# Kernel tuning notes

Measured on AMD Instinct MI355X. Metric: run time of the kernel, lower is better.

The kernel has to match this reference:

```python
import jax, jax.numpy as jnp
import numpy as np

# IO parameters (aihwkit-style preset)
INP_BOUND = 1.0
INP_RES = 1.0 / 254.0      # 8-bit DAC: 2^8 - 2 levels
OUT_BOUND = 12.0
OUT_RES = 1.0 / 510.0      # 9-bit ADC: 2^9 - 2 levels
OUT_NOISE = 0.06
OUT_SCALE = 1.0
MAX_BM_FACTOR = 1000.0
MAX_BM_RES = 0.25
INP_RES_EFF = 2.0 * INP_BOUND * INP_RES  # effective input grid step (bm escape test)


def _quantize_st(x, res, bound):
    # UniformQuantize: round to grid of step (res * 2 * bound), straight-through grad
    r = (1.0 / res if res > 1.0 else res) * 2.0 * bound
    q = jnp.round(x / r) * r
    return x + jax.lax.stop_gradient(q - x)


def _one_pass(input_, weight, nm, reduction, rnd, key):
    """One analog MVM pass at a given bound-management reduction factor."""
    scale = 1.0 / (nm * reduction)                      # [m, 1]
    x = input_ * scale                                  # noise/bound managed input
    x = _quantize_st(x, INP_RES, INP_BOUND)             # DAC discretization
    x = jnp.clip(x, -INP_BOUND, INP_BOUND)              # DAC clipping
    out = x @ weight.T                                  # [m, out_size] analog GEMM
    noise = OUT_NOISE * jax.random.normal(
        jax.random.fold_in(key, rnd), out.shape, out.dtype)
    out = out + noise                                   # output (ADC) noise
    out = _quantize_st(out, OUT_RES, OUT_BOUND)         # ADC discretization
    not_clipping = jnp.all((out <= OUT_BOUND) & (out >= -OUT_BOUND))
    out = jnp.clip(out, -OUT_BOUND, OUT_BOUND)          # ADC saturation
    return not_clipping, out


def setup_inputs() -> dict:
    key = jax.random.key(0)
    k1, k2 = jax.random.split(key)
    input_ = jax.random.normal(k1, (8192, 4096), jnp.float32)
    # 0.1 std weights -> outputs mostly within ADC bound after 1-2 bm rounds
    weight = 0.1 * jax.random.normal(k2, (4096, 4096), jnp.float32)
    return {"input_": input_, "weight": weight}


def reference(input_, weight):
    key = jax.random.key(42)
    # noise management: ABS_MAX over the input dimension (nm_thres <= 0 -> no clamp)
    nm = jnp.max(jnp.abs(input_), axis=-1, keepdims=True)
    nm = jnp.where(nm <= 0.0, 1.0, nm)
    out_shape = input_.shape[:-1] + (weight.shape[0],)

    def cond(c):
        return ~c[2]

    def body(c):
        rnd, red, _, _ = c
        red = red * 2.0          # reduction_due_to_bound_management *= 2
        rnd = rnd + 1
        passed, out = _one_pass(input_, weight, nm, red, rnd, key)
        passed = passed | (red > MAX_BM_FACTOR) | (red > MAX_BM_RES / INP_RES_EFF)
        return (rnd, red, passed, out)

    init = (jnp.int32(0), jnp.float32(0.5), jnp.array(False),
            jnp.zeros(out_shape, input_.dtype))
    _, red, _, out = jax.lax.while_loop(cond, body, init)
    # undo the input scaling: output *= out_scale / scale = out_scale * nm * red
    return out * (OUT_SCALE * nm * red)
```

## Files before the change

kernel.cpp:

```cpp
#include <hip/hip_runtime.h>
#include <stdint.h>


#define MM 8192
#define KK 4096
#define NN 4096
#define TOTAL_OUT ((size_t)MM * (size_t)NN)
#define GEMM_BLOCKS 2048

typedef __attribute__((ext_vector_type(4))) float f32x4;
typedef __attribute__((ext_vector_type(8))) short bf16x8;
typedef __attribute__((ext_vector_type(8))) unsigned short u16x8;

#define R_IN_F ((float)(2.0 / 254.0))
#define R_OUT_F ((float)(24.0 / 510.0))

struct BmState {
  int done;
  float red_final;
  int viol[8];
  int ctr[8];
};

__host__ __device__ __forceinline__ uint32_t tf_rotl(uint32_t v, int r) {
  return (v << r) | (v >> (32 - r));
}

__host__ __device__ __forceinline__ void threefry2x32(uint32_t k0, uint32_t k1,
                                                      uint32_t x0, uint32_t x1,
                                                      uint32_t &o0, uint32_t &o1) {
  uint32_t ks2 = k0 ^ k1 ^ 0x1BD11BDAu;
  x0 += k0; x1 += k1;
#define TF_R(r) { x0 += x1; x1 = tf_rotl(x1, r); x1 ^= x0; }
  TF_R(13) TF_R(15) TF_R(26) TF_R(6)
  x0 += k1; x1 += ks2 + 1u;
  TF_R(17) TF_R(29) TF_R(16) TF_R(24)
  x0 += ks2; x1 += k0 + 2u;
  TF_R(13) TF_R(15) TF_R(26) TF_R(6)
  x0 += k0; x1 += k1 + 3u;
  TF_R(17) TF_R(29) TF_R(16) TF_R(24)
  x0 += k1; x1 += ks2 + 4u;
  TF_R(13) TF_R(15) TF_R(26) TF_R(6)
  x0 += ks2; x1 += k0 + 5u;
#undef TF_R
  o0 = x0; o1 = x1;
}

__device__ __forceinline__ float erfinv_xla(float x) {
  float w = -log1pf(-x * x);
  float p;
  if (w < 5.0f) {
    w = w - 2.5f;
    p = 2.81022636e-08f;
    p = fmaf(p, w, 3.43273939e-07f);
    p = fmaf(p, w, -3.5233877e-06f);
    p = fmaf(p, w, -4.39150654e-06f);
    p = fmaf(p, w, 0.00021858087f);
    p = fmaf(p, w, -0.00125372503f);
    p = fmaf(p, w, -0.00417768164f);
    p = fmaf(p, w, 0.246640727f);
    p = fmaf(p, w, 1.50140941f);
  } else {
    w = sqrtf(w) - 3.0f;
    p = -0.000200214257f;
    p = fmaf(p, w, 0.000100950558f);
    p = fmaf(p, w, 0.00134934322f);
    p = fmaf(p, w, -0.00367342844f);
    p = fmaf(p, w, 0.00573950773f);
    p = fmaf(p, w, -0.0076224613f);
    p = fmaf(p, w, 0.00943887047f);
    p = fmaf(p, w, 1.00167406f);
    p = fmaf(p, w, 2.83297682f);
  }
  return p * x;
}

__device__ __forceinline__ float noise_from_bits(uint32_t bits) {
  uint32_t fb = (bits >> 9) | 0x3f800000u;
  float f = __uint_as_float(fb) - 1.0f;
  const float lo = -0.99999994f;
  float u = f * 2.0f + lo;
  u = fmaxf(lo, u);
  return 0.06f * (1.41421356f * erfinv_xla(u));
}

__device__ __forceinline__ unsigned short bf16_rne(float f) {
  uint32_t x = __float_as_uint(f);
  x += 0x7fffu + ((x >> 16) & 1u);
  return (unsigned short)(x >> 16);
}

__device__ __forceinline__ float dac_quant(float v, float s) {
  float x = v * s;
  float t = x / R_IN_F;
  float k = rintf(t);
  return fminf(127.0f, fmaxf(-127.0f, k));
}

__device__ __forceinline__ u16x8 quant8(float4 a, float4 b, float s) {
  u16x8 o;
  o[0] = bf16_rne(dac_quant(a.x, s));
  o[1] = bf16_rne(dac_quant(a.y, s));
  o[2] = bf16_rne(dac_quant(a.z, s));
  o[3] = bf16_rne(dac_quant(a.w, s));
  o[4] = bf16_rne(dac_quant(b.x, s));
  o[5] = bf16_rne(dac_quant(b.y, s));
  o[6] = bf16_rne(dac_quant(b.z, s));
  o[7] = bf16_rne(dac_quant(b.w, s));
  return o;
}

__device__ __forceinline__ u16x8 conv8(float4 a, float4 b) {
  u16x8 o;
  o[0] = bf16_rne(a.x); o[1] = bf16_rne(a.y); o[2] = bf16_rne(a.z); o[3] = bf16_rne(a.w);
  o[4] = bf16_rne(b.x); o[5] = bf16_rne(b.y); o[6] = bf16_rne(b.z); o[7] = bf16_rne(b.w);
  return o;
}

__device__ __forceinline__ float adc_one(float gval, size_t idx, float sc,
                                         uint32_t fk0, uint32_t fk1, bool &bad) {
  uint32_t w0, w1;
  threefry2x32(fk0, fk1, 0u, (uint32_t)idx, w0, w1);
  float o = R_IN_F * gval + noise_from_bits(w0 ^ w1);
  float q = rintf(o / R_OUT_F) * R_OUT_F;
  float z = o + (q - o);
  bad = bad || (z > 12.0f) || (z < -12.0f);
  z = fminf(12.0f, fmaxf(-12.0f, z));
  return z * sc;
}

__device__ __forceinline__ void fin_tail(BmState *st, int pass, float red, int nblocks,
                                         bool bad) {
  unsigned long long vb = __ballot(bad ? 1 : 0);
  if (vb != 0ull && (threadIdx.x & 63) == 0) atomicOr(&st->viol[pass], 1);
  __syncthreads();
  if (threadIdx.x == 0) {
    __threadfence();
    int prev = atomicAdd(&st->ctr[pass], 1);
    if (prev == nblocks - 1) {
      int viol = atomicOr(&st->viol[pass], 0);
      bool ok = (viol == 0) || (red > 1000.0f) || (red > 31.75f);
      if (ok) {
        st->done = 1;
        st->red_final = red;
      }
    }
  }
}

__global__ __launch_bounds__(256) void k_rowmax(const float *__restrict__ in,
                                                float *__restrict__ nm, BmState *st) {
  if (blockIdx.x == 0 && threadIdx.x == 0) {
    st->done = 0;
    st->red_final = 0.0f;
    for (int i = 0; i < 8; ++i) { st->viol[i] = 0; st->ctr[i] = 0; }
  }
  const int row = blockIdx.x;
  const float4 *r = (const float4 *)(in + (size_t)row * KK);
  const int t = threadIdx.x;
  float m = 0.0f;
#pragma unroll
  for (int i = 0; i < 4; ++i) {
    float4 v = r[t + i * 256];
    m = fmaxf(m, fmaxf(fmaxf(fabsf(v.x), fabsf(v.y)), fmaxf(fabsf(v.z), fabsf(v.w))));
  }
#pragma unroll
  for (int off = 32; off > 0; off >>= 1) m = fmaxf(m, __shfl_down(m, off));
  __shared__ float wm[4];
  if ((t & 63) == 0) wm[t >> 6] = m;
  __syncthreads();
  if (t == 0) {
    m = fmaxf(fmaxf(wm[0], wm[1]), fmaxf(wm[2], wm[3]));
    nm[row] = (m <= 0.0f) ? 1.0f : m;
  }
}

__global__ __launch_bounds__(256) void k_wconv(const float *__restrict__ w,
                                               unsigned short *__restrict__ wb) {
  const size_t idx = ((size_t)blockIdx.x * 256 + threadIdx.x) * 8;
  float4 a = *(const float4 *)(w + idx);
  float4 b = *(const float4 *)(w + idx + 4);
  *(u16x8 *)(wb + idx) = conv8(a, b);
}

__global__ __launch_bounds__(256) void k_quant(const float *__restrict__ in,
                                               const float *__restrict__ nm,
                                               unsigned short *__restrict__ ab) {
  const size_t idx = ((size_t)blockIdx.x * 256 + threadIdx.x) * 8;
  const int row = (int)(idx >> 12);
  const float s = 1.0f / (nm[row] * 1.0f);
  float4 a = *(const float4 *)(in + idx);
  float4 b = *(const float4 *)(in + idx + 4);
  *(u16x8 *)(ab + idx) = quant8(a, b, s);
}

__device__ __forceinline__ void async16(const void *g, void *l) {
  __builtin_amdgcn_global_load_lds((const __attribute__((address_space(1))) uint32_t *)g,
                                   (__attribute__((address_space(3))) uint32_t *)l,
                                   16, 0, 0);
}

__global__ __launch_bounds__(256) void k_gemm(const unsigned short *__restrict__ A,
                                              const unsigned short *__restrict__ B,
                                              float *__restrict__ C) {
  __shared__ unsigned short As[128 * 64];
  __shared__ unsigned short Bs[128 * 64];
  const int tid = threadIdx.x;
  const int lane = tid & 63;
  const int wv = tid >> 6;
  const int wr = wv >> 1, wc = wv & 1;
  const int brow = blockIdx.y * 128;
  const int bcol = blockIdx.x * 128;

  f32x4 acc[4][4];
#pragma unroll
  for (int m = 0; m < 4; ++m)
#pragma unroll
    for (int n = 0; n < 4; ++n) acc[m][n] = (f32x4){0.f, 0.f, 0.f, 0.f};

  for (int kt = 0; kt < KK; kt += 64) {
#pragma unroll
    for (int i = 0; i < 4; ++i) {
      const int u0 = i * 256 + wv * 64;
      const int u = u0 + lane;
      const int r = u >> 3;
      const int cg = (u & 7) ^ (r & 7);
      const int k8 = cg * 8;
      async16(A + (size_t)(brow + r) * KK + kt + k8, (char *)As + (size_t)u0 * 16);
      async16(B + (size_t)(bcol + r) * KK + kt + k8, (char *)Bs + (size_t)u0 * 16);
    }
    __syncthreads();

    const int r16 = lane & 15;
    const int kg = (lane >> 4) * 8;
#pragma unroll
    for (int kk = 0; kk < 64; kk += 32) {
      const int ck = (kk + kg) >> 3;
      bf16x8 af[4], bg[4];
#pragma unroll
      for (int m = 0; m < 4; ++m) {
        const int ra = wr * 64 + m * 16 + r16;
        af[m] = *(const bf16x8 *)(As + ra * 64 + ((ck ^ (ra & 7)) << 3));
      }
#pragma unroll
      for (int n = 0; n < 4; ++n) {
        const int rb = wc * 64 + n * 16 + r16;
        bg[n] = *(const bf16x8 *)(Bs + rb * 64 + ((ck ^ (rb & 7)) << 3));
      }
#pragma unroll
      for (int m = 0; m < 4; ++m)
#pragma unroll
        for (int n = 0; n < 4; ++n)
          acc[m][n] = __builtin_amdgcn_mfma_f32_16x16x32_bf16(af[m], bg[n], acc[m][n], 0, 0, 0);
    }
    __syncthreads();
  }

  const int c16 = lane & 15;
  const int q4 = (lane >> 4) * 4;
#pragma unroll
  for (int m = 0; m < 4; ++m) {
    const int row = brow + wr * 64 + m * 16 + q4;
#pragma unroll
    for (int n = 0; n < 4; ++n) {
      const int col = bcol + wc * 64 + n * 16 + c16;
      float *cp = C + (size_t)row * NN + col;
      cp[0 * (size_t)NN] = acc[m][n][0];
      cp[1 * (size_t)NN] = acc[m][n][1];
      cp[2 * (size_t)NN] = acc[m][n][2];
      cp[3 * (size_t)NN] = acc[m][n][3];
    }
  }
}

__global__ __launch_bounds__(256) void k_epi(float *__restrict__ out,
                                             const float *__restrict__ nm,
                                             BmState *__restrict__ st, int pass, float red,
                                             uint32_t fk0, uint32_t fk1) {
  const size_t idx = ((size_t)blockIdx.x * 256 + threadIdx.x) * 8;
  const int row = (int)(idx >> 12);
  const float sc = nm[row] * red;
  float4 a = *(const float4 *)(out + idx);
  float4 b = *(const float4 *)(out + idx + 4);
  float v[8] = {a.x, a.y, a.z, a.w, b.x, b.y, b.z, b.w};
  bool bad = false;
#pragma unroll
  for (int j = 0; j < 8; ++j) v[j] = adc_one(v[j], idx + j, sc, fk0, fk1, bad);
  *(float4 *)(out + idx) = make_float4(v[0], v[1], v[2], v[3]);
  *(float4 *)(out + idx + 4) = make_float4(v[4], v[5], v[6], v[7]);
  unsigned long long vb = __ballot(bad ? 1 : 0);
  if (vb != 0ull && (threadIdx.x & 63) == 0) atomicOr(&st->viol[pass], 1);
}

__global__ void k_fin(BmState *st, int pass, float red) {
  if (st->done) return;
  bool ok = (st->viol[pass] == 0) || (red > 1000.0f) || (red > 31.75f);
  if (ok) {
    st->done = 1;
    st->red_final = red;
  }
}

__global__ __launch_bounds__(256) void k_retry(const float *__restrict__ Af,
                                               const float *__restrict__ Bf,
                                               const float *__restrict__ nm, float red,
                                               float *__restrict__ C,
                                               BmState *__restrict__ st, int pass,
                                               uint32_t fk0, uint32_t fk1) {
  if (st->done) return;
  __shared__ unsigned short As[128 * 64];
  __shared__ unsigned short Bs[128 * 64];
  const int tid = threadIdx.x;
  const int lane = tid & 63;
  const int wv = tid >> 6;
  const int wr = wv >> 1, wc = wv & 1;
  const int brow = blockIdx.y * 128;
  const int bcol = blockIdx.x * 128;

  f32x4 acc[4][4];
#pragma unroll
  for (int m = 0; m < 4; ++m)
#pragma unroll
    for (int n = 0; n < 4; ++n) acc[m][n] = (f32x4){0.f, 0.f, 0.f, 0.f};

  float sA[4];
#pragma unroll
  for (int i = 0; i < 4; ++i) {
    int u = i * 256 + tid;
    sA[i] = 1.0f / (nm[brow + (u >> 3)] * red);
  }

  for (int kt = 0; kt < KK; kt += 64) {
#pragma unroll
    for (int i = 0; i < 4; ++i) {
      const int u = i * 256 + tid;
      const int r = u >> 3, k8 = (u & 7) * 8;
      {
        const float *g = Af + (size_t)(brow + r) * KK + kt + k8;
        float4 x = *(const float4 *)g, y = *(const float4 *)(g + 4);
        *(u16x8 *)(As + r * 64 + k8) = quant8(x, y, sA[i]);
      }
      {
        const float *g = Bf + (size_t)(bcol + r) * KK + kt + k8;
        float4 x = *(const float4 *)g, y = *(const float4 *)(g + 4);
        *(u16x8 *)(Bs + r * 64 + k8) = conv8(x, y);
      }
    }
    __syncthreads();

    const int r16 = lane & 15;
    const int kg = (lane >> 4) * 8;
#pragma unroll
    for (int kk = 0; kk < 64; kk += 32) {
      bf16x8 af[4], bg[4];
#pragma unroll
      for (int m = 0; m < 4; ++m)
        af[m] = *(const bf16x8 *)(As + (wr * 64 + m * 16 + r16) * 64 + kk + kg);
#pragma unroll
      for (int n = 0; n < 4; ++n)
        bg[n] = *(const bf16x8 *)(Bs + (wc * 64 + n * 16 + r16) * 64 + kk + kg);
#pragma unroll
      for (int m = 0; m < 4; ++m)
#pragma unroll
        for (int n = 0; n < 4; ++n)
          acc[m][n] = __builtin_amdgcn_mfma_f32_16x16x32_bf16(af[m], bg[n], acc[m][n], 0, 0, 0);
    }
    __syncthreads();
  }

  const int c16 = lane & 15;
  const int q4 = (lane >> 4) * 4;
  bool bad = false;
#pragma unroll
  for (int m = 0; m < 4; ++m) {
    const int row0 = brow + wr * 64 + m * 16 + q4;
#pragma unroll
    for (int j = 0; j < 4; ++j) {
      const int row = row0 + j;
      const float sc = nm[row] * red;
#pragma unroll
      for (int n = 0; n < 4; ++n) {
        const int col = bcol + wc * 64 + n * 16 + c16;
        const size_t idx = (size_t)row * NN + col;
        C[idx] = adc_one(acc[m][n][j], idx, sc, fk0, fk1, bad);
      }
    }
  }
  fin_tail(st, pass, red, GEMM_BLOCKS, bad);
}

extern "C" void kernel_launch(void *const *d_in, const int *in_sizes, int n_in,
                              void *d_out, int out_size, void *d_ws, size_t ws_size,
                              hipStream_t stream) {
  const float *input = (const float *)d_in[0];
  const float *weight = (const float *)d_in[1];
  if (n_in >= 2 && in_sizes[0] < in_sizes[1]) {
    const float *t = input; input = weight; weight = t;
  }
  float *out = (float *)d_out;
  char *ws = (char *)d_ws;
  BmState *st = (BmState *)ws;
  float *nm = (float *)(ws + 4096);
  unsigned short *Ab = (unsigned short *)(ws + 36864);
  unsigned short *Wb = Ab + (size_t)MM * KK;
  const size_t need = 36864 + ((size_t)MM * KK + (size_t)NN * KK) * 2;
  const bool fast = ws_size >= need;

  uint32_t fk[8][2];
  for (int p = 1; p <= 6; ++p) threefry2x32(0u, 42u, 0u, (uint32_t)p, fk[p][0], fk[p][1]);

  k_rowmax<<<dim3(MM), dim3(256), 0, stream>>>(input, nm, st);

  if (fast) {
    k_wconv<<<dim3((NN * (size_t)KK) / 2048), dim3(256), 0, stream>>>(weight, Wb);
    k_quant<<<dim3((MM * (size_t)KK) / 2048), dim3(256), 0, stream>>>(input, nm, Ab);
    k_gemm<<<dim3(NN / 128, MM / 128), dim3(256), 0, stream>>>(Ab, Wb, out);
    k_epi<<<dim3((int)(TOTAL_OUT / 2048)), dim3(256), 0, stream>>>(out, nm, st, 1, 1.0f,
                                                                   fk[1][0], fk[1][1]);
    k_fin<<<dim3(1), dim3(1), 0, stream>>>(st, 1, 1.0f);
  } else {
    k_retry<<<dim3(NN / 128, MM / 128), dim3(256), 0, stream>>>(
        input, weight, nm, 1.0f, out, st, 1, fk[1][0], fk[1][1]);
  }

  float red = 2.0f;
  for (int p = 2; p <= 6; ++p, red *= 2.0f) {
    k_retry<<<dim3(NN / 128, MM / 128), dim3(256), 0, stream>>>(
        input, weight, nm, red, out, st, p, fk[p][0], fk[p][1]);
  }
}
```

Before: 557.0 us.

## Double-buffer GEMM LDS tiles and fuse row-max with input quantization

The GEMM now keeps two LDS buffers for A and B. It issues the async global-to-LDS loads for the next K tile before computing the current one, using explicit vmcnt waits and barriers, so load latency is hidden behind the MFMA work. The separate row-max and quantize kernels are also merged into one per-row kernel that reads each input row once, which removes one full pass over the input and one launch. The cost is double the LDS per block, which may reduce occupancy, plus more fragile hand-written wait-count synchronization.

```diff
diff --git a/kernel.cpp b/kernel.cpp
--- a/kernel.cpp
+++ b/kernel.cpp
@@ -7,6 +7,7 @@
 #define NN 4096
 #define TOTAL_OUT ((size_t)MM * (size_t)NN)
 #define GEMM_BLOCKS 2048
+#define NT (KK / 64)
 
 typedef __attribute__((ext_vector_type(4))) float f32x4;
 typedef __attribute__((ext_vector_type(8))) short bf16x8;
@@ -148,6 +149,41 @@
   }
 }
 
+__global__ __launch_bounds__(256) void k_rowquant(const float *__restrict__ in,
+                                                  float *__restrict__ nm,
+                                                  unsigned short *__restrict__ ab,
+                                                  BmState *st) {
+  if (blockIdx.x == 0 && threadIdx.x == 0) {
+    st->done = 0;
+    st->red_final = 0.0f;
+    for (int i = 0; i < 8; ++i) { st->viol[i] = 0; st->ctr[i] = 0; }
+  }
+  const int row = blockIdx.x;
+  const float *r = in + (size_t)row * KK;
+  const int t = threadIdx.x;
+  float4 a0 = *(const float4 *)(r + t * 8);
+  float4 a1 = *(const float4 *)(r + t * 8 + 4);
+  float4 b0 = *(const float4 *)(r + 2048 + t * 8);
+  float4 b1 = *(const float4 *)(r + 2048 + t * 8 + 4);
+  float m = 0.0f;
+  m = fmaxf(m, fmaxf(fmaxf(fabsf(a0.x), fabsf(a0.y)), fmaxf(fabsf(a0.z), fabsf(a0.w))));
+  m = fmaxf(m, fmaxf(fmaxf(fabsf(a1.x), fabsf(a1.y)), fmaxf(fabsf(a1.z), fabsf(a1.w))));
+  m = fmaxf(m, fmaxf(fmaxf(fabsf(b0.x), fabsf(b0.y)), fmaxf(fabsf(b0.z), fabsf(b0.w))));
+  m = fmaxf(m, fmaxf(fmaxf(fabsf(b1.x), fabsf(b1.y)), fmaxf(fabsf(b1.z), fabsf(b1.w))));
+#pragma unroll
+  for (int off = 32; off > 0; off >>= 1) m = fmaxf(m, __shfl_down(m, off));
+  __shared__ float wm[4];
+  if ((t & 63) == 0) wm[t >> 6] = m;
+  __syncthreads();
+  const float mm = fmaxf(fmaxf(wm[0], wm[1]), fmaxf(wm[2], wm[3]));
+  const float nmv = (mm <= 0.0f) ? 1.0f : mm;
+  if (t == 0) nm[row] = nmv;
+  const float s = 1.0f / (nmv * 1.0f);
+  unsigned short *o = ab + (size_t)row * KK;
+  *(u16x8 *)(o + t * 8) = quant8(a0, a1, s);
+  *(u16x8 *)(o + 2048 + t * 8) = quant8(b0, b1, s);
+}
+
 __global__ __launch_bounds__(256) void k_rowmax(const float *__restrict__ in,
                                                 float *__restrict__ nm, BmState *st) {
   if (blockIdx.x == 0 && threadIdx.x == 0) {
@@ -183,17 +219,6 @@
   *(u16x8 *)(wb + idx) = conv8(a, b);
 }
 
-__global__ __launch_bounds__(256) void k_quant(const float *__restrict__ in,
-                                               const float *__restrict__ nm,
-                                               unsigned short *__restrict__ ab) {
-  const size_t idx = ((size_t)blockIdx.x * 256 + threadIdx.x) * 8;
-  const int row = (int)(idx >> 12);
-  const float s = 1.0f / (nm[row] * 1.0f);
-  float4 a = *(const float4 *)(in + idx);
-  float4 b = *(const float4 *)(in + idx + 4);
-  *(u16x8 *)(ab + idx) = quant8(a, b, s);
-}
-
 __device__ __forceinline__ void async16(const void *g, void *l) {
   __builtin_amdgcn_global_load_lds((const __attribute__((address_space(1))) uint32_t *)g,
                                    (__attribute__((address_space(3))) uint32_t *)l,
@@ -203,8 +228,8 @@
 __global__ __launch_bounds__(256) void k_gemm(const unsigned short *__restrict__ A,
                                               const unsigned short *__restrict__ B,
                                               float *__restrict__ C) {
-  __shared__ unsigned short As[128 * 64];
-  __shared__ unsigned short Bs[128 * 64];
+  __shared__ unsigned short As[2][128 * 64];
+  __shared__ unsigned short Bs[2][128 * 64];
   const int tid = threadIdx.x;
   const int lane = tid & 63;
   const int wv = tid >> 6;
@@ -218,21 +243,42 @@
 #pragma unroll
     for (int n = 0; n < 4; ++n) acc[m][n] = (f32x4){0.f, 0.f, 0.f, 0.f};
 
-  for (int kt = 0; kt < KK; kt += 64) {
-#pragma unroll
-    for (int i = 0; i < 4; ++i) {
-      const int u0 = i * 256 + wv * 64;
-      const int u = u0 + lane;
-      const int r = u >> 3;
-      const int cg = (u & 7) ^ (r & 7);
-      const int k8 = cg * 8;
-      async16(A + (size_t)(brow + r) * KK + kt + k8, (char *)As + (size_t)u0 * 16);
-      async16(B + (size_t)(bcol + r) * KK + kt + k8, (char *)Bs + (size_t)u0 * 16);
-    }
-    __syncthreads();
-
-    const int r16 = lane & 15;
-    const int kg = (lane >> 4) * 8;
+  const int su0[4] = {0 * 256 + wv * 64, 1 * 256 + wv * 64, 2 * 256 + wv * 64,
+                      3 * 256 + wv * 64};
+  int sr[4], sk8[4];
+#pragma unroll
+  for (int i = 0; i < 4; ++i) {
+    const int u = su0[i] + lane;
+    sr[i] = u >> 3;
+    sk8[i] = ((u & 7) ^ (sr[i] & 7)) * 8;
+  }
+
+#define STAGE(buf, kt)                                                                 \
+  {                                                                                    \
+    _Pragma("unroll") for (int i = 0; i < 4; ++i) {                                    \
+      async16(A + (size_t)(brow + sr[i]) * KK + (kt) * 64 + sk8[i],                    \
+              (char *)As[buf] + (size_t)su0[i] * 16);                                  \
+      async16(B + (size_t)(bcol + sr[i]) * KK + (kt) * 64 + sk8[i],                    \
+              (char *)Bs[buf] + (size_t)su0[i] * 16);                                  \
+    }                                                                                  \
+  }
+
+  STAGE(0, 0);
+
+  const int r16 = lane & 15;
+  const int kg = (lane >> 4) * 8;
+
+#pragma unroll 2
+  for (int kt = 0; kt < NT; ++kt) {
+    const int cur = kt & 1;
+    if (kt + 1 < NT) {
+      STAGE(cur ^ 1, kt + 1);
+      asm volatile("s_waitcnt vmcnt(8)" ::: "memory");
+    } else {
+      asm volatile("s_waitcnt vmcnt(0)" ::: "memory");
+    }
+    __builtin_amdgcn_s_barrier();
+
 #pragma unroll
     for (int kk = 0; kk < 64; kk += 32) {
       const int ck = (kk + kg) >> 3;
@@ -240,12 +286,12 @@
 #pragma unroll
       for (int m = 0; m < 4; ++m) {
         const int ra = wr * 64 + m * 16 + r16;
-        af[m] = *(const bf16x8 *)(As + ra * 64 + ((ck ^ (ra & 7)) << 3));
+        af[m] = *(const bf16x8 *)(As[cur] + ra * 64 + ((ck ^ (ra & 7)) << 3));
       }
 #pragma unroll
       for (int n = 0; n < 4; ++n) {
         const int rb = wc * 64 + n * 16 + r16;
-        bg[n] = *(const bf16x8 *)(Bs + rb * 64 + ((ck ^ (rb & 7)) << 3));
+        bg[n] = *(const bf16x8 *)(Bs[cur] + rb * 64 + ((ck ^ (rb & 7)) << 3));
       }
 #pragma unroll
       for (int m = 0; m < 4; ++m)
@@ -253,8 +299,10 @@
         for (int n = 0; n < 4; ++n)
           acc[m][n] = __builtin_amdgcn_mfma_f32_16x16x32_bf16(af[m], bg[n], acc[m][n], 0, 0, 0);
     }
-    __syncthreads();
-  }
+    __builtin_amdgcn_sched_barrier(0);
+    __builtin_amdgcn_s_barrier();
+  }
+#undef STAGE
 
   const int c16 = lane & 15;
   const int q4 = (lane >> 4) * 4;
@@ -409,16 +457,15 @@
   uint32_t fk[8][2];
   for (int p = 1; p <= 6; ++p) threefry2x32(0u, 42u, 0u, (uint32_t)p, fk[p][0], fk[p][1]);
 
-  k_rowmax<<<dim3(MM), dim3(256), 0, stream>>>(input, nm, st);
-
   if (fast) {
+    k_rowquant<<<dim3(MM), dim3(256), 0, stream>>>(input, nm, Ab, st);
     k_wconv<<<dim3((NN * (size_t)KK) / 2048), dim3(256), 0, stream>>>(weight, Wb);
-    k_quant<<<dim3((MM * (size_t)KK) / 2048), dim3(256), 0, stream>>>(input, nm, Ab);
     k_gemm<<<dim3(NN / 128, MM / 128), dim3(256), 0, stream>>>(Ab, Wb, out);
     k_epi<<<dim3((int)(TOTAL_OUT / 2048)), dim3(256), 0, stream>>>(out, nm, st, 1, 1.0f,
                                                                    fk[1][0], fk[1][1]);
     k_fin<<<dim3(1), dim3(1), 0, stream>>>(st, 1, 1.0f);
   } else {
+    k_rowmax<<<dim3(MM), dim3(256), 0, stream>>>(input, nm, st);
     k_retry<<<dim3(NN / 128, MM / 128), dim3(256), 0, stream>>>(
         input, weight, nm, 1.0f, out, st, 1, fk[1][0], fk[1][1]);
   }
```

Result: faster. 531.4 us (-4.6%).
